# Performance work log

Measured on AMD Instinct MI355X. Metric: run time of the kernel, lower is better.

The kernel has to match this reference:

```python
import jax, jax.numpy as jnp
import numpy as np

TEMPERATURE = 8.0  # sqrt(d_k) with d_k = 64
NEG_INF = -jnp.inf


def setup_inputs() -> dict:
    key = jax.random.key(0)
    kq, kk, kv = jax.random.split(key, 3)
    b, n, d = 16, 2048, 64
    q = jax.random.normal(kq, (b, n, d), dtype=jnp.float32)
    k = jax.random.normal(kk, (b, n, d), dtype=jnp.float32)
    v = jax.random.normal(kv, (b, n, d), dtype=jnp.float32)
    # causal mask: True where attention is disallowed (strict upper triangle)
    mask = jnp.broadcast_to(jnp.triu(jnp.ones((n, n), dtype=bool), k=1), (b, n, n))
    return {"q": q, "k": k, "v": v, "mask": mask}


def reference(q, k, v, mask):
    # attn = q @ k^T / temperature   [b, n, n]
    attn = jnp.einsum('bqd,bkd->bqk', q, k) / TEMPERATURE
    attn = jnp.where(mask, NEG_INF, attn)
    attn = jax.nn.softmax(attn, axis=2)
    # output = attn @ v   [b, n, d]
    output = jnp.einsum('bqk,bkd->bqd', attn, v)
    return (output, attn)
```

## Files before the change

### kernel.cpp

```cpp
#include <hip/hip_runtime.h>


constexpr int B = 16;
constexpr int N = 2048;
constexpr int D = 64;
constexpr float INV_TEMP = 0.125f;

constexpr int RS = 2056;
constexpr int SP_BYTES  = 32 * RS * 2;
constexpr int SK_OFF    = SP_BYTES;
constexpr int SV_OFF    = SK_OFF + 64 * 72 * 2;
constexpr int RSUM_OFF  = SV_OFF + 64 * 72 * 2;
constexpr int SINV_OFF  = RSUM_OFF + 8 * 16 * 4;
constexpr int SMEM_BYTES = SINV_OFF + 32 * 4;

typedef __attribute__((ext_vector_type(8))) short bf16x8;
typedef __attribute__((ext_vector_type(4))) short bf16x4;
typedef __attribute__((ext_vector_type(4))) float f32x4;

__device__ __forceinline__ short f2bf(float f) {
    __bf16 h = (__bf16)f;
    return __builtin_bit_cast(short, h);
}
__device__ __forceinline__ float bf2f(short s) {
    unsigned int u = ((unsigned int)(unsigned short)s) << 16;
    return __builtin_bit_cast(float, u);
}

__global__ __launch_bounds__(512) void sdpa_fused(
    const float* __restrict__ q,
    const float* __restrict__ k,
    const float* __restrict__ v,
    float* __restrict__ out,
    float* __restrict__ attn)
{
    extern __shared__ __align__(16) char smem[];
    short (*sP)[RS] = reinterpret_cast<short(*)[RS]>(smem);
    short (*sK)[72] = reinterpret_cast<short(*)[72]>(smem + SK_OFF);
    short (*sV)[72] = reinterpret_cast<short(*)[72]>(smem + SV_OFF);
    float* rsum = reinterpret_cast<float*>(smem + RSUM_OFF);
    float* sinv = reinterpret_cast<float*>(smem + SINV_OFF);

    const int x = blockIdx.x;
    const int b = x >> 6;
    const int u = x & 63;
    const int rt = 63 - u;
    const int qs = rt * 32;
    const int ntiles = (rt >> 1) + 1;

    const int t    = threadIdx.x;
    const int w    = t >> 6;
    const int lane = t & 63;
    const int l15  = lane & 15;
    const int quad = lane >> 4;
    const int q8   = quad * 8;
    const int rg   = w & 1;
    const int cg   = w >> 1;

    const float* qb = q + (size_t)b * N * D;
    const float* kb = k + (size_t)b * N * D;
    const float* vb = v + (size_t)b * N * D;
    float* attn_b = attn + (size_t)b * N * N;

    const int krow = t >> 3;
    const int kc8  = (t & 7) * 8;

    float4 kf0, kf1;
    float  vr[8];

    {
        const float4* s = (const float4*)(kb + (size_t)krow * D + kc8);
        kf0 = s[0]; kf1 = s[1];
        const float* sv = vb + (size_t)(w * 8) * D + lane;
#pragma unroll
        for (int i = 0; i < 8; ++i) vr[i] = sv[(size_t)i * D];
    }

    if (t < 256) {
        const float4* s = (const float4*)(qb + (size_t)(qs + krow) * D + kc8);
        float4 a = s[0], c4 = s[1];
        float qv[8] = {a.x,a.y,a.z,a.w, c4.x,c4.y,c4.z,c4.w};
        bf16x8 pq;
#pragma unroll
        for (int i = 0; i < 8; ++i) pq[i] = f2bf(qv[i]);
        *(bf16x8*)&sK[krow][kc8] = pq;
    }
    __syncthreads();
    const bf16x8 qa0 = *(const bf16x8*)&sK[rg * 16 + l15][q8];
    const bf16x8 qa1 = *(const bf16x8*)&sK[rg * 16 + l15][32 + q8];

    float rs[4] = {0.f, 0.f, 0.f, 0.f};
    f32x4 o = {0.f, 0.f, 0.f, 0.f};

    for (int kt = 0; kt < ntiles; ++kt) {
        __syncthreads();
        {
            float kv[8] = {kf0.x,kf0.y,kf0.z,kf0.w, kf1.x,kf1.y,kf1.z,kf1.w};
            bf16x8 pk, pv;
#pragma unroll
            for (int i = 0; i < 8; ++i) pk[i] = f2bf(kv[i]);
#pragma unroll
            for (int i = 0; i < 8; ++i) pv[i] = f2bf(vr[i]);
            *(bf16x8*)&sK[krow][kc8]  = pk;
            *(bf16x8*)&sV[lane][w*8]  = pv;
        }
        __syncthreads();
        if (kt + 1 < ntiles) {
            const float4* s = (const float4*)(kb + (size_t)((kt+1)*64 + krow) * D + kc8);
            kf0 = s[0]; kf1 = s[1];
            const float* sv = vb + (size_t)((kt+1)*64 + w*8) * D + lane;
#pragma unroll
            for (int i = 0; i < 8; ++i) vr[i] = sv[(size_t)i * D];
        }
        bf16x8 kb0 = *(const bf16x8*)&sK[cg * 16 + l15][q8];
        bf16x8 kb1 = *(const bf16x8*)&sK[cg * 16 + l15][32 + q8];
        f32x4 c = {0.f, 0.f, 0.f, 0.f};
        c = __builtin_amdgcn_mfma_f32_16x16x32_bf16(qa0, kb0, c, 0, 0, 0);
        c = __builtin_amdgcn_mfma_f32_16x16x32_bf16(qa1, kb1, c, 0, 0, 0);
        const int colg = kt * 64 + cg * 16 + l15;
#pragma unroll
        for (int r = 0; r < 4; ++r) {
            const int rowg = qs + rg * 16 + quad * 4 + r;
            float pr = (colg <= rowg) ? __expf(c[r] * INV_TEMP) : 0.f;
            short sp = f2bf(pr);
            rs[r] += bf2f(sp);
            sP[rg * 16 + quad * 4 + r][kt * 64 + cg * 16 + l15] = sp;
        }
        __syncthreads();
#pragma unroll
        for (int kc = 0; kc < 2; ++kc) {
            bf16x8 a  = *(const bf16x8*)&sP[rg * 16 + l15][kt * 64 + kc * 32 + q8];
            bf16x8 vf = *(const bf16x8*)&sV[cg * 16 + l15][kc * 32 + q8];
            o = __builtin_amdgcn_mfma_f32_16x16x32_bf16(a, vf, o, 0, 0, 0);
        }
    }

#pragma unroll
    for (int r = 0; r < 4; ++r) {
        float s = rs[r];
        s += __shfl_xor(s, 1);
        s += __shfl_xor(s, 2);
        s += __shfl_xor(s, 4);
        s += __shfl_xor(s, 8);
        rs[r] = s;
    }
    if (l15 == 0) {
#pragma unroll
        for (int r = 0; r < 4; ++r) rsum[w * 16 + quad * 4 + r] = rs[r];
    }
    __syncthreads();
    if (t < 32) {
        const int rg2 = t >> 4, rl = t & 15;
        float tot = rsum[(rg2 + 0) * 16 + rl] + rsum[(rg2 + 2) * 16 + rl]
                  + rsum[(rg2 + 4) * 16 + rl] + rsum[(rg2 + 6) * 16 + rl];
        sinv[t] = 1.f / tot;
    }
    __syncthreads();

#pragma unroll
    for (int r = 0; r < 4; ++r) {
        const int rowl = rg * 16 + quad * 4 + r;
        out[(size_t)(b * N + qs + rowl) * D + cg * 16 + l15] = o[r] * sinv[rowl];
    }

    const int erow = t >> 4;
    const int ec   = (t & 15) * 4;
    const float einv = sinv[erow];
    float* arow = attn_b + (size_t)(qs + erow) * N;
    const int lim = ntiles * 64;
    for (int c0 = ec; c0 < N; c0 += 64) {
        float4 f;
        if (c0 < lim) {
            bf16x4 p4 = *(const bf16x4*)&sP[erow][c0];
            f.x = bf2f(p4[0]) * einv;
            f.y = bf2f(p4[1]) * einv;
            f.z = bf2f(p4[2]) * einv;
            f.w = bf2f(p4[3]) * einv;
        } else {
            f = {0.f, 0.f, 0.f, 0.f};
        }
        *(float4*)(arow + c0) = f;
    }
}

extern "C" void kernel_launch(void* const* d_in, const int* in_sizes, int n_in,
                              void* d_out, int out_size, void* d_ws, size_t ws_size,
                              hipStream_t stream) {
    const float* q = (const float*)d_in[0];
    const float* k = (const float*)d_in[1];
    const float* v = (const float*)d_in[2];

    float* out  = (float*)d_out;
    float* attn = out + (size_t)B * N * D;

    static bool attr_set = false;
    if (!attr_set) {
        (void)hipFuncSetAttribute((const void*)sdpa_fused,
                                  hipFuncAttributeMaxDynamicSharedMemorySize,
                                  SMEM_BYTES);
        attr_set = true;
    }

    sdpa_fused<<<dim3(B * 64), dim3(512), SMEM_BYTES, stream>>>(q, k, v, out, attn);
}
```

Measured before the change: 514.1 us.

## Split into flash-style output kernel and separate attention-matrix recompute kernel

Replaces the single fused kernel, which held a 32x2048 bf16 probability tile in shared memory, with two kernels. The first keeps only a 64-column P tile in LDS, computes the output and row sums, and writes the inverse row sums to workspace. The second recomputes QK^T, exponentiates, normalizes with the stored inverse and writes the attention matrix, including the zero tail, straight to global memory. This frees large LDS so more blocks fit per CU, at the cost of recomputing the scores, an extra launch and a global round trip for the inverse sums. Row sums now accumulate in fp32 rather than rounded bf16.

```diff
diff --git a/kernel.cpp b/kernel.cpp
--- a/kernel.cpp
+++ b/kernel.cpp
@@ -6,40 +6,26 @@
 constexpr int D = 64;
 constexpr float INV_TEMP = 0.125f;
 
-constexpr int RS = 2056;
-constexpr int SP_BYTES  = 32 * RS * 2;
-constexpr int SK_OFF    = SP_BYTES;
-constexpr int SV_OFF    = SK_OFF + 64 * 72 * 2;
-constexpr int RSUM_OFF  = SV_OFF + 64 * 72 * 2;
-constexpr int SINV_OFF  = RSUM_OFF + 8 * 16 * 4;
-constexpr int SMEM_BYTES = SINV_OFF + 32 * 4;
-
 typedef __attribute__((ext_vector_type(8))) short bf16x8;
-typedef __attribute__((ext_vector_type(4))) short bf16x4;
 typedef __attribute__((ext_vector_type(4))) float f32x4;
 
 __device__ __forceinline__ short f2bf(float f) {
     __bf16 h = (__bf16)f;
     return __builtin_bit_cast(short, h);
 }
-__device__ __forceinline__ float bf2f(short s) {
-    unsigned int u = ((unsigned int)(unsigned short)s) << 16;
-    return __builtin_bit_cast(float, u);
-}
-
-__global__ __launch_bounds__(512) void sdpa_fused(
+
+__global__ __launch_bounds__(512) void sdpa_flash(
     const float* __restrict__ q,
     const float* __restrict__ k,
     const float* __restrict__ v,
     float* __restrict__ out,
-    float* __restrict__ attn)
+    float* __restrict__ invws)
 {
-    extern __shared__ __align__(16) char smem[];
-    short (*sP)[RS] = reinterpret_cast<short(*)[RS]>(smem);
-    short (*sK)[72] = reinterpret_cast<short(*)[72]>(smem + SK_OFF);
-    short (*sV)[72] = reinterpret_cast<short(*)[72]>(smem + SV_OFF);
-    float* rsum = reinterpret_cast<float*>(smem + RSUM_OFF);
-    float* sinv = reinterpret_cast<float*>(smem + SINV_OFF);
+    __shared__ __align__(16) short sK[64][72];
+    __shared__ __align__(16) short sV[64][72];
+    __shared__ __align__(16) short sPt[32][72];
+    __shared__ float rsum[128];
+    __shared__ float sinv[32];
 
     const int x = blockIdx.x;
     const int b = x >> 6;
@@ -60,7 +46,6 @@
     const float* qb = q + (size_t)b * N * D;
     const float* kb = k + (size_t)b * N * D;
     const float* vb = v + (size_t)b * N * D;
-    float* attn_b = attn + (size_t)b * N * N;
 
     const int krow = t >> 3;
     const int kc8  = (t & 7) * 8;
@@ -112,24 +97,23 @@
 #pragma unroll
             for (int i = 0; i < 8; ++i) vr[i] = sv[(size_t)i * D];
         }
-        bf16x8 kb0 = *(const bf16x8*)&sK[cg * 16 + l15][q8];
-        bf16x8 kb1 = *(const bf16x8*)&sK[cg * 16 + l15][32 + q8];
+        bf16x8 b0 = *(const bf16x8*)&sK[cg * 16 + l15][q8];
+        bf16x8 b1 = *(const bf16x8*)&sK[cg * 16 + l15][32 + q8];
         f32x4 c = {0.f, 0.f, 0.f, 0.f};
-        c = __builtin_amdgcn_mfma_f32_16x16x32_bf16(qa0, kb0, c, 0, 0, 0);
-        c = __builtin_amdgcn_mfma_f32_16x16x32_bf16(qa1, kb1, c, 0, 0, 0);
+        c = __builtin_amdgcn_mfma_f32_16x16x32_bf16(qa0, b0, c, 0, 0, 0);
+        c = __builtin_amdgcn_mfma_f32_16x16x32_bf16(qa1, b1, c, 0, 0, 0);
         const int colg = kt * 64 + cg * 16 + l15;
 #pragma unroll
         for (int r = 0; r < 4; ++r) {
             const int rowg = qs + rg * 16 + quad * 4 + r;
             float pr = (colg <= rowg) ? __expf(c[r] * INV_TEMP) : 0.f;
-            short sp = f2bf(pr);
-            rs[r] += bf2f(sp);
-            sP[rg * 16 + quad * 4 + r][kt * 64 + cg * 16 + l15] = sp;
+            rs[r] += pr;
+            sPt[rg * 16 + quad * 4 + r][cg * 16 + l15] = f2bf(pr);
         }
         __syncthreads();
 #pragma unroll
         for (int kc = 0; kc < 2; ++kc) {
-            bf16x8 a  = *(const bf16x8*)&sP[rg * 16 + l15][kt * 64 + kc * 32 + q8];
+            bf16x8 a  = *(const bf16x8*)&sPt[rg * 16 + l15][kc * 32 + q8];
             bf16x8 vf = *(const bf16x8*)&sV[cg * 16 + l15][kc * 32 + q8];
             o = __builtin_amdgcn_mfma_f32_16x16x32_bf16(a, vf, o, 0, 0, 0);
         }
@@ -154,6 +138,7 @@
         float tot = rsum[(rg2 + 0) * 16 + rl] + rsum[(rg2 + 2) * 16 + rl]
                   + rsum[(rg2 + 4) * 16 + rl] + rsum[(rg2 + 6) * 16 + rl];
         sinv[t] = 1.f / tot;
+        invws[(size_t)b * N + qs + t] = sinv[t];
     }
     __syncthreads();
 
@@ -162,24 +147,90 @@
         const int rowl = rg * 16 + quad * 4 + r;
         out[(size_t)(b * N + qs + rowl) * D + cg * 16 + l15] = o[r] * sinv[rowl];
     }
-
+}
+
+__global__ __launch_bounds__(512) void sdpa_attn(
+    const float* __restrict__ q,
+    const float* __restrict__ k,
+    const float* __restrict__ attn_unused,
+    float* __restrict__ attn,
+    const float* __restrict__ invws)
+{
+    __shared__ __align__(16) short sQ[32][72];
+    __shared__ float sinv[32];
+
+    const int x = blockIdx.x;
+    const int b = x >> 6;
+    const int u = x & 63;
+    const int rt = 63 - u;
+    const int qs = rt * 32;
+    const int ntiles = (rt >> 1) + 1;
+
+    const int t    = threadIdx.x;
+    const int w    = t >> 6;
+    const int lane = t & 63;
+    const int l15  = lane & 15;
+    const int quad = lane >> 4;
+    const int q8   = quad * 8;
+    const int rg   = w & 1;
+    const int cg   = w >> 1;
+
+    const float* qb = q + (size_t)b * N * D;
+    const float* kb = k + (size_t)b * N * D;
+    float* attn_b = attn + (size_t)b * N * N;
+
+    if (t < 256) {
+        const int krow = t >> 3, kc8 = (t & 7) * 8;
+        const float4* s = (const float4*)(qb + (size_t)(qs + krow) * D + kc8);
+        float4 a = s[0], c4 = s[1];
+        float qv[8] = {a.x,a.y,a.z,a.w, c4.x,c4.y,c4.z,c4.w};
+        bf16x8 pq;
+#pragma unroll
+        for (int i = 0; i < 8; ++i) pq[i] = f2bf(qv[i]);
+        *(bf16x8*)&sQ[krow][kc8] = pq;
+    }
+    if (t >= 256 && t < 288) sinv[t - 256] = invws[(size_t)b * N + qs + (t - 256)];
+    __syncthreads();
+
+    const bf16x8 qa0 = *(const bf16x8*)&sQ[rg * 16 + l15][q8];
+    const bf16x8 qa1 = *(const bf16x8*)&sQ[rg * 16 + l15][32 + q8];
+
+    const int qrow = qs + rg * 16 + l15;
+    const float einv = sinv[rg * 16 + l15];
+    float* arow = attn_b + (size_t)qrow * N;
+
+    for (int kt = 0; kt < ntiles; ++kt) {
+        const float* kr = kb + (size_t)(kt * 64 + cg * 16 + l15) * D;
+        const float4* kp = (const float4*)(kr + q8);
+        float4 k0 = kp[0], k1 = kp[1];
+        const float4* kp2 = (const float4*)(kr + 32 + q8);
+        float4 k2 = kp2[0], k3 = kp2[1];
+        float kv[16] = {k0.x,k0.y,k0.z,k0.w, k1.x,k1.y,k1.z,k1.w,
+                        k2.x,k2.y,k2.z,k2.w, k3.x,k3.y,k3.z,k3.w};
+        bf16x8 kb0, kb1;
+#pragma unroll
+        for (int i = 0; i < 8; ++i) { kb0[i] = f2bf(kv[i]); kb1[i] = f2bf(kv[8 + i]); }
+
+        f32x4 c = {0.f, 0.f, 0.f, 0.f};
+        c = __builtin_amdgcn_mfma_f32_16x16x32_bf16(kb0, qa0, c, 0, 0, 0);
+        c = __builtin_amdgcn_mfma_f32_16x16x32_bf16(kb1, qa1, c, 0, 0, 0);
+
+        const int kg0 = kt * 64 + cg * 16 + quad * 4;
+        float4 pv;
+        pv.x = (kg0 + 0 <= qrow) ? __expf(c[0] * INV_TEMP) * einv : 0.f;
+        pv.y = (kg0 + 1 <= qrow) ? __expf(c[1] * INV_TEMP) * einv : 0.f;
+        pv.z = (kg0 + 2 <= qrow) ? __expf(c[2] * INV_TEMP) * einv : 0.f;
+        pv.w = (kg0 + 3 <= qrow) ? __expf(c[3] * INV_TEMP) * einv : 0.f;
+        *(float4*)(arow + kg0) = pv;
+    }
+
+    const int lim  = ntiles * 64;
     const int erow = t >> 4;
     const int ec   = (t & 15) * 4;
-    const float einv = sinv[erow];
-    float* arow = attn_b + (size_t)(qs + erow) * N;
-    const int lim = ntiles * 64;
-    for (int c0 = ec; c0 < N; c0 += 64) {
-        float4 f;
-        if (c0 < lim) {
-            bf16x4 p4 = *(const bf16x4*)&sP[erow][c0];
-            f.x = bf2f(p4[0]) * einv;
-            f.y = bf2f(p4[1]) * einv;
-            f.z = bf2f(p4[2]) * einv;
-            f.w = bf2f(p4[3]) * einv;
-        } else {
-            f = {0.f, 0.f, 0.f, 0.f};
-        }
-        *(float4*)(arow + c0) = f;
+    float* zrow = attn_b + (size_t)(qs + erow) * N;
+    const float4 z = {0.f, 0.f, 0.f, 0.f};
+    for (int c0 = lim + ec; c0 < N; c0 += 64) {
+        *(float4*)(zrow + c0) = z;
     }
 }
 
@@ -192,14 +243,8 @@
 
     float* out  = (float*)d_out;
     float* attn = out + (size_t)B * N * D;
-
-    static bool attr_set = false;
-    if (!attr_set) {
-        (void)hipFuncSetAttribute((const void*)sdpa_fused,
-                                  hipFuncAttributeMaxDynamicSharedMemorySize,
-                                  SMEM_BYTES);
-        attr_set = true;
-    }
-
-    sdpa_fused<<<dim3(B * 64), dim3(512), SMEM_BYTES, stream>>>(q, k, v, out, attn);
-}
+    float* invws = (float*)d_ws;
+
+    sdpa_flash<<<dim3(B * 64), dim3(512), 0, stream>>>(q, k, v, out, invws);
+    sdpa_attn <<<dim3(B * 64), dim3(512), 0, stream>>>(q, k, attn, attn, invws);
+}
```

New measurement: 536.2 us. +4.3%, slower.
